# Kernel optimization log

Hardware: AMD Instinct MI355X
Metric: run time of the kernel (lower is better)

## Reference

```python
import jax, jax.numpy as jnp
import numpy as np

B, N, DIM = 8, 512, 768
H, DH = 12, 64
INNER = H * DH
MLP = 3072
DEPTH = 4
EPS = 1e-5
LS = 0.1  # LayerScale init_eps for depth <= 18


def _ln(x, scale):
    # flax LayerNorm(use_bias=False): (x-mean)/sqrt(var+eps) * scale
    mu = jnp.mean(x, axis=-1, keepdims=True)
    var = jnp.mean(jnp.square(x - mu), axis=-1, keepdims=True)
    return (x - mu) * jax.lax.rsqrt(var + EPS) * scale


def setup_inputs() -> dict:
    key = jax.random.key(0)
    ks = jax.random.split(key, 13)
    s = 0.02
    inp = {
        "x": jax.random.normal(ks[0], (B, N, DIM), jnp.float32),
        "ln1": jnp.ones((DEPTH, DIM), jnp.float32),
        "Wq": jax.random.normal(ks[1], (DEPTH, DIM, INNER), jnp.float32) * s,
        "Wkv": jax.random.normal(ks[2], (DEPTH, DIM, 2 * INNER), jnp.float32) * s,
        "mix_pre": jax.random.normal(ks[3], (DEPTH, H, H), jnp.float32) * 0.1,
        "mix_post": jax.random.normal(ks[4], (DEPTH, H, H), jnp.float32) * 0.1,
        "Wo": jax.random.normal(ks[5], (DEPTH, INNER, DIM), jnp.float32) * s,
        "bo": jnp.zeros((DEPTH, DIM), jnp.float32),
        "ln2": jnp.ones((DEPTH, DIM), jnp.float32),
        "W1": jax.random.normal(ks[6], (DEPTH, DIM, MLP), jnp.float32) * s,
        "b1": jnp.zeros((DEPTH, MLP), jnp.float32),
        "W2": jax.random.normal(ks[7], (DEPTH, MLP, DIM), jnp.float32) * s,
        "b2": jnp.zeros((DEPTH, DIM), jnp.float32),
    }
    return inp


def _block(x, p):
    ln1, Wq, Wkv, mp, mq, Wo, bo, ln2, W1, b1, W2, b2 = p
    scale = DH ** -0.5
    h = _ln(x, ln1)
    q = h @ Wq                                  # [b,n,inner]
    kv = h @ Wkv
    k, v = jnp.split(kv, 2, axis=-1)
    def to_heads(t):
        return t.reshape(B, N, H, DH).transpose(0, 2, 1, 3)  # b h n d
    q, k, v = to_heads(q), to_heads(k), to_heads(v)
    dots = jnp.einsum('bhid,bhjd->bhij', q, k) * scale
    dots = jnp.einsum('bhij,hg->bgij', dots, mp)   # talking-heads pre-softmax
    attn = jax.nn.softmax(dots, axis=-1)
    attn = jnp.einsum('bhij,hg->bgij', attn, mq)   # talking-heads post-softmax
    o = jnp.einsum('bhij,bhjd->bhid', attn, v)
    o = o.transpose(0, 2, 1, 3).reshape(B, N, INNER)
    x = (o @ Wo + bo) * LS + x
    h2 = _ln(x, ln2)
    x = ((jax.nn.gelu(h2 @ W1 + b1) @ W2) + b2) * LS + x
    return x, None


def reference(x, ln1, Wq, Wkv, mix_pre, mix_post, Wo, bo, ln2, W1, b1, W2, b2):
    params = (ln1, Wq, Wkv, mix_pre, mix_post, Wo, bo, ln2, W1, b1, W2, b2)
    out, _ = jax.lax.scan(_block, x, params)
    return out
```

## Files before the change

### kernel.cpp

```cpp
#include <hip/hip_runtime.h>


#define LSCALE 0.1f

typedef __bf16 bf16;
typedef __bf16 bf16x8 __attribute__((ext_vector_type(8)));
typedef __bf16 bf16x4 __attribute__((ext_vector_type(4)));
typedef unsigned short ushort4v __attribute__((ext_vector_type(4)));
typedef float  f32x4  __attribute__((ext_vector_type(4)));

__device__ __forceinline__ void g2l16(const void* g, void* l) {
    __builtin_amdgcn_global_load_lds(
        (const __attribute__((address_space(1))) void*)g,
        (__attribute__((address_space(3))) void*)l, 16, 0, 0);
}

template<int EPI, bool PLANA = false>
__global__ __launch_bounds__(256, 2)
void gemm_bt(const bf16* __restrict__ A, int lda, long saz1, long saz2,
             const bf16* __restrict__ Bt, int ldb, long sbz1, long sbz2,
             void* __restrict__ Cv, int ldc, long scz1, long scz2,
             int M, int N, int K, int zmod,
             const float* __restrict__ bias, float scale)
{
    __shared__ __align__(16) char smem[35840];
    bf16* As = (bf16*)smem;
    bf16* Bs = (bf16*)(smem + 16384);
    bf16* Cs = (bf16*)smem;

    const int z  = blockIdx.z;
    const int z1 = z / zmod, z2 = z - z1 * zmod;
    const bf16* Ab = A  + saz1 * (long)z1 + saz2 * (long)z2;
    const bf16* Bb = Bt + sbz1 * (long)z1 + sbz2 * (long)z2;

    const int m0 = blockIdx.x * 128, n0 = blockIdx.y * 128;
    const int tid = threadIdx.x, w = tid >> 6, l = tid & 63;
    const int wr = (w >> 1) * 64, wc = (w & 1) * 64;
    const int lr = l & 15, lq = l >> 4;
    const int srow = l >> 2, scol8 = (l & 3) * 8;

    long abase = 0;
    if constexpr (PLANA)
        abase = (long)(m0 >> 9) * 393216 + (long)((m0 & 511) + w * 32) * 64;

    f32x4 acc[4][4];
#pragma unroll
    for (int i = 0; i < 4; i++)
#pragma unroll
        for (int j = 0; j < 4; j++)
#pragma unroll
            for (int r = 0; r < 4; r++) acc[i][j][r] = 0.f;

    for (int k0 = 0; k0 < K; k0 += 64) {
        const bf16* Ag;
        int ldaa;
        if constexpr (PLANA) {
            Ag = Ab + abase + ((long)(k0 >> 6)) * 32768;
            ldaa = 64;
        } else {
            Ag = Ab + (long)(m0 + w * 32) * lda + k0;
            ldaa = lda;
        }
        const bf16* Bg = Bb + (long)(n0 + w * 32) * ldb + k0;
        g2l16(Ag + (long)srow * ldaa + scol8,             As + w * 1024);
        g2l16(Ag + (long)(srow + 16) * ldaa + scol8,      As + w * 1024 + 512);
        g2l16(Ag + (long)srow * ldaa + 32 + scol8,        As + 4096 + w * 1024);
        g2l16(Ag + (long)(srow + 16) * ldaa + 32 + scol8, As + 4096 + w * 1024 + 512);
        g2l16(Bg + (long)srow * ldb + scol8,             Bs + w * 1024);
        g2l16(Bg + (long)(srow + 16) * ldb + scol8,      Bs + w * 1024 + 512);
        g2l16(Bg + (long)srow * ldb + 32 + scol8,        Bs + 4096 + w * 1024);
        g2l16(Bg + (long)(srow + 16) * ldb + 32 + scol8, Bs + 4096 + w * 1024 + 512);
        __syncthreads();

#pragma unroll
        for (int hh = 0; hh < 2; hh++) {
            bf16x8 fa[4], fb[4];
#pragma unroll
            for (int i = 0; i < 4; i++)
                fa[i] = *(const bf16x8*)(As + hh * 4096 + (wr + i * 16 + lr) * 32 + lq * 8);
#pragma unroll
            for (int i = 0; i < 4; i++)
                fb[i] = *(const bf16x8*)(Bs + hh * 4096 + (wc + i * 16 + lr) * 32 + lq * 8);
#pragma unroll
            for (int mi = 0; mi < 4; mi++)
#pragma unroll
                for (int ni = 0; ni < 4; ni++)
                    acc[mi][ni] = __builtin_amdgcn_mfma_f32_16x16x32_bf16(
                        fa[mi], fb[ni], acc[mi][ni], 0, 0, 0);
        }
        __syncthreads();
    }

#pragma unroll
    for (int ni = 0; ni < 4; ni++) {
        const int col = wc + ni * 16 + lr;
        float bv = 0.f;
        if (EPI == 1) bv = bias[n0 + col];
#pragma unroll
        for (int mi = 0; mi < 4; mi++) {
#pragma unroll
            for (int r = 0; r < 4; r++) {
                const int row = wr + mi * 16 + lq * 4 + r;
                float v = acc[mi][ni][r];
                if (EPI == 0) {
                    v *= scale;
                } else if (EPI == 1) {
                    const float xx = v + bv;
                    const float u  = 0.7978845608f * (xx + 0.044715f * xx * xx * xx);
                    const float th = 1.f - 2.f / (__expf(2.f * u) + 1.f);
                    v = 0.5f * xx * (1.f + th);
                }
                Cs[row * 136 + col] = (bf16)v;
            }
        }
    }
    __syncthreads();

    const long cb = scz1 * (long)z1 + scz2 * (long)z2;
    const int rrow = tid >> 4, cg = tid & 15;
#pragma unroll
    for (int p = 0; p < 8; p++) {
        const int row = p * 16 + rrow;
        const bf16x8 v = *(const bf16x8*)(Cs + row * 136 + cg * 8);
        *(bf16x8*)((bf16*)Cv + cb + (long)(m0 + row) * ldc + n0 + cg * 8) = v;
    }
}

template<int PLANO>
__global__ __launch_bounds__(256, 4)
void gemm_av(const bf16* __restrict__ S, const bf16* __restrict__ qkvc,
             bf16* __restrict__ oc)
{
    __shared__ __align__(16) char av_smem[9728];
    bf16* As  = (bf16*)av_smem;
    bf16* Bst = (bf16*)(av_smem + 4096);
    bf16* Cs  = (bf16*)av_smem;

    const int z = blockIdx.y, b = z / 12, g = z - b * 12;
    const bf16* Ab = S + (long)z * 262144;
    const bf16* Bb = qkvc + (long)b * 1179648 + 1536 + g * 64;

    const int i0 = blockIdx.x * 64;
    const int tid = threadIdx.x, w = tid >> 6, l = tid & 63;
    const int lr = l & 15, lq = l >> 4;
    const int srow = l >> 2, scol8 = (l & 3) * 8;
    const int kp = tid >> 4, dq = tid & 15;
    const int kcol = ((((kp >> 2) ^ ((dq >> 1) & 3)) << 3) | ((kp & 3) << 1));

    f32x4 acc[4];
#pragma unroll
    for (int j = 0; j < 4; j++)
#pragma unroll
        for (int r = 0; r < 4; r++) acc[j][r] = 0.f;

    unsigned short* Bw = (unsigned short*)Bst;

    for (int k0 = 0; k0 < 512; k0 += 32) {
        const bf16* Ag = Ab + (long)(i0 + w * 16) * 512 + k0;
        g2l16(Ag + (long)srow * 512 + scol8, As + w * 512);

        const bf16* Bg = Bb + (long)(k0 + 2 * kp) * 2304 + dq * 4;
        ushort4v u0 = *(const ushort4v*)(Bg);
        ushort4v u1 = *(const ushort4v*)(Bg + 2304);
#pragma unroll
        for (int r = 0; r < 4; r++) {
            unsigned p = (unsigned)u0[r] | ((unsigned)u1[r] << 16);
            *(unsigned*)(Bw + (dq * 4 + r) * 40 + kcol) = p;
        }
        __syncthreads();

        bf16x8 fa = *(const bf16x8*)(As + (w * 16 + lr) * 32 + lq * 8);
        bf16x8 fb[4];
#pragma unroll
        for (int i = 0; i < 4; i++) {
            const int d = i * 16 + lr;
            fb[i] = *(const bf16x8*)(Bst + d * 40 + ((lq ^ ((d >> 3) & 3)) << 3));
        }
#pragma unroll
        for (int ni = 0; ni < 4; ni++)
            acc[ni] = __builtin_amdgcn_mfma_f32_16x16x32_bf16(
                fa, fb[ni], acc[ni], 0, 0, 0);
        __syncthreads();
    }

    if constexpr (PLANO) {
#pragma unroll
        for (int ni = 0; ni < 4; ni++)
#pragma unroll
            for (int r = 0; r < 4; r++)
                Cs[(w * 16 + lq * 4 + r) * 68 + ni * 16 + lr] = (bf16)acc[ni][r];
        __syncthreads();
        const int rr = tid >> 2, c16 = (tid & 3) * 16;
        bf16* orow = oc + ((long)z * 512 + i0 + rr) * 64 + c16;
        *(bf16x8*)(orow)     = *(const bf16x8*)(Cs + rr * 68 + c16);
        *(bf16x8*)(orow + 8) = *(const bf16x8*)(Cs + rr * 68 + c16 + 8);
    } else {
        bf16* Cb = oc + (long)b * 1179648 + g * 64;
#pragma unroll
        for (int ni = 0; ni < 4; ni++) {
            const int gc = ni * 16 + lr;
#pragma unroll
            for (int r = 0; r < 4; r++) {
                const int gr = i0 + w * 16 + lq * 4 + r;
                Cb[(long)gr * 2304 + gc] = (bf16)acc[ni][r];
            }
        }
    }
}

__global__ __launch_bounds__(256)
void tconv_k(const float* __restrict__ in, bf16* __restrict__ out,
             int K, int N)
{
    __shared__ float t[32][33];
    const int n0 = blockIdx.x * 32, k0 = blockIdx.y * 32;
    const int x = threadIdx.x, y = threadIdx.y;
#pragma unroll
    for (int yy = 0; yy < 4; yy++)
        t[y + yy * 8][x] = in[(long)(k0 + y + yy * 8) * N + n0 + x];
    __syncthreads();
#pragma unroll
    for (int yy = 0; yy < 4; yy++)
        out[(long)(n0 + y + yy * 8) * K + k0 + x] = (bf16)t[x][y + yy * 8];
}

__global__ __launch_bounds__(256)
void pre_k(const float* __restrict__ Wq, const float* __restrict__ Wkv,
           const float* __restrict__ Wo, const float* __restrict__ W1,
           const float* __restrict__ W2, bf16* __restrict__ WtAll,
           const float* __restrict__ x, float* __restrict__ xf,
           const float* __restrict__ gam, bf16* __restrict__ hout)
{
    __shared__ __align__(16) char pmem[16640];
    const int bxg = blockIdx.x;
    const int t = threadIdx.x;
    if (bxg < 6912) {
        float (*st)[65] = (float(*)[65])pmem;
        const int L = bxg / 1728;
        int bx = bxg - L * 1728;
        bf16* WtL = WtAll + (long)L * 7077888;
        const float* src; bf16* dst; int K, N, ntn;
        if (bx < 144) {
            src = Wq + (long)L * 589824;   dst = WtL;            K = 768;  N = 768;  ntn = 12;
        } else if (bx < 432) {
            bx -= 144;
            src = Wkv + (long)L * 1179648; dst = WtL + 589824;   K = 768;  N = 1536; ntn = 24;
        } else if (bx < 576) {
            bx -= 432;
            src = Wo + (long)L * 589824;   dst = WtL + 1769472;  K = 768;  N = 768;  ntn = 12;
        } else if (bx < 1152) {
            bx -= 576;
            src = W1 + (long)L * 2359296;  dst = WtL + 2359296;  K = 768;  N = 3072; ntn = 48;
        } else {
            bx -= 1152;
            src = W2 + (long)L * 2359296;  dst = WtL + 4718592;  K = 3072; N = 768;  ntn = 12;
        }
        const int n0 = (bx % ntn) * 64, k0 = (bx / ntn) * 64;
        const int r = t >> 4, c4 = (t & 15) * 4;
#pragma unroll
        for (int rr = 0; rr < 4; rr++) {
            const f32x4 v = *(const f32x4*)(src + (long)(k0 + r + rr * 16) * N + n0 + c4);
            st[r + rr * 16][c4 + 0] = v[0];
            st[r + rr * 16][c4 + 1] = v[1];
            st[r + rr * 16][c4 + 2] = v[2];
            st[r + rr * 16][c4 + 3] = v[3];
        }
        __syncthreads();
        const int kc = (t & 7) * 8;
#pragma unroll
        for (int p = 0; p < 2; p++) {
            const int n = p * 32 + (t >> 3);
            bf16x8 o;
#pragma unroll
            for (int e = 0; e < 8; e++) o[e] = (bf16)st[kc + e][n];
            *(bf16x8*)(dst + (long)(n0 + n) * K + k0 + kc) = o;
        }
    } else {
        const int row = bxg - 6912;
        float* ps  = (float*)pmem;
        float* pss = (float*)pmem + 4;
        const float* xin = x + (long)row * 768;
        float* xr = xf + (long)row * 768;
        float v[3];
#pragma unroll
        for (int i = 0; i < 3; i++) {
            const int c = t + i * 256;
            const float xv = xin[c];
            xr[c] = xv;
            v[i] = xv;
        }
        float s  = v[0] + v[1] + v[2];
        float ss = v[0] * v[0] + v[1] * v[1] + v[2] * v[2];
#pragma unroll
        for (int off = 32; off; off >>= 1) {
            s  += __shfl_xor(s, off);
            ss += __shfl_xor(ss, off);
        }
        const int wv = t >> 6, l = t & 63;
        if (l == 0) { ps[wv] = s; pss[wv] = ss; }
        __syncthreads();
        s  = ps[0] + ps[1] + ps[2] + ps[3];
        ss = pss[0] + pss[1] + pss[2] + pss[3];
        const float mu = s * (1.f / 768.f);
        const float rs = rsqrtf(ss * (1.f / 768.f) - mu * mu + 1e-5f);
        bf16* orow = hout + (long)row * 768;
#pragma unroll
        for (int i = 0; i < 3; i++) {
            const int c = t + i * 256;
            orow[c] = (bf16)((v[i] - mu) * rs * gam[c]);
        }
    }
}

__global__ __launch_bounds__(256)
void lnres_k(float* __restrict__ xf, const bf16* __restrict__ P0,
             const bf16* __restrict__ P1, const float* __restrict__ bias,
             const float* __restrict__ gam, bf16* __restrict__ out,
             const float* __restrict__ src)
{
    const int row = blockIdx.x, t = threadIdx.x;
    float* xr = xf + (long)row * 768;
    float v[3];
#pragma unroll
    for (int i = 0; i < 3; i++) {
        const int c = t + i * 256;
        float xv;
        if (src) {
            xv = src[(long)row * 768 + c];
            xr[c] = xv;
        } else if (P0) {
            xv = xr[c] + LSCALE * ((float)P0[(long)row * 768 + c] +
                                   (float)P1[(long)row * 768 + c] + bias[c]);
            xr[c] = xv;
        } else {
            xv = xr[c];
        }
        v[i] = xv;
    }
    float s  = v[0] + v[1] + v[2];
    float ss = v[0] * v[0] + v[1] * v[1] + v[2] * v[2];
#pragma unroll
    for (int off = 32; off; off >>= 1) {
        s  += __shfl_xor(s, off);
        ss += __shfl_xor(ss, off);
    }
    __shared__ float ps[4], pss[4];
    const int wv = t >> 6, l = t & 63;
    if (l == 0) { ps[wv] = s; pss[wv] = ss; }
    __syncthreads();
    s  = ps[0] + ps[1] + ps[2] + ps[3];
    ss = pss[0] + pss[1] + pss[2] + pss[3];
    const float mu = s * (1.f / 768.f);
    const float rs = rsqrtf(ss * (1.f / 768.f) - mu * mu + 1e-5f);
    bf16* orow = out + (long)row * 768;
#pragma unroll
    for (int i = 0; i < 3; i++) {
        const int c = t + i * 256;
        orow[c] = (bf16)((v[i] - mu) * rs * gam[c]);
    }
}

__global__ __launch_bounds__(256)
void outres_k(const float* __restrict__ xf, const bf16* __restrict__ P0,
              const bf16* __restrict__ P1, const float* __restrict__ bias,
              float* __restrict__ out)
{
    const long i4 = ((long)blockIdx.x * 256 + threadIdx.x) * 4;
    const int c = (int)(i4 % 768);
    const f32x4 xv = *(const f32x4*)(xf + i4);
    const bf16x4 p0 = *(const bf16x4*)(P0 + i4);
    const bf16x4 p1 = *(const bf16x4*)(P1 + i4);
    const f32x4 bv = *(const f32x4*)(bias + c);
    f32x4 o;
#pragma unroll
    for (int e = 0; e < 4; e++)
        o[e] = xv[e] + LSCALE * ((float)p0[e] + (float)p1[e] + bv[e]);
    *(f32x4*)(out + i4) = o;
}

__global__ __launch_bounds__(256)
void mixsm_k(bf16* __restrict__ S, const float* __restrict__ mp,
             const float* __restrict__ mq)
{
    const int b = blockIdx.y, i4 = blockIdx.x, t = threadIdx.x;
    const int w = t >> 6, l = t & 63;
    const int row = i4 * 4 + w;
    bf16* Sb = S + ((long)b * 12 * 512 + row) * 512 + l * 8;

    float a[12][8];
#pragma unroll
    for (int g = 0; g < 12; g++)
#pragma unroll
        for (int e = 0; e < 8; e++) a[g][e] = 0.f;

#pragma unroll
    for (int h = 0; h < 12; h++) {
        const bf16x8 sv = *(const bf16x8*)(Sb + (long)h * 262144);
        float f[8];
#pragma unroll
        for (int e = 0; e < 8; e++) f[e] = (float)sv[e];
#pragma unroll
        for (int g = 0; g < 12; g++) {
            const float m = mp[h * 12 + g];
#pragma unroll
            for (int e = 0; e < 8; e++) a[g][e] += f[e] * m;
        }
    }

#pragma unroll
    for (int g = 0; g < 12; g++) {
        float mx = a[g][0];
#pragma unroll
        for (int e = 1; e < 8; e++) mx = fmaxf(mx, a[g][e]);
#pragma unroll
        for (int off = 32; off; off >>= 1) mx = fmaxf(mx, __shfl_xor(mx, off));
        float sm = 0.f;
#pragma unroll
        for (int e = 0; e < 8; e++) {
            const float ev = __expf(a[g][e] - mx);
            a[g][e] = ev;
            sm += ev;
        }
#pragma unroll
        for (int off = 32; off; off >>= 1) sm += __shfl_xor(sm, off);
        const float rd = 1.f / sm;
#pragma unroll
        for (int e = 0; e < 8; e++) a[g][e] *= rd;
    }

#pragma unroll
    for (int hf = 0; hf < 2; hf++) {
        float o[6][8];
#pragma unroll
        for (int gg = 0; gg < 6; gg++)
#pragma unroll
            for (int e = 0; e < 8; e++) o[gg][e] = 0.f;
#pragma unroll
        for (int h = 0; h < 12; h++) {
#pragma unroll
            for (int gg = 0; gg < 6; gg++) {
                const float m = mq[h * 12 + hf * 6 + gg];
#pragma unroll
                for (int e = 0; e < 8; e++) o[gg][e] += a[h][e] * m;
            }
        }
#pragma unroll
        for (int gg = 0; gg < 6; gg++) {
            bf16x8 ov;
#pragma unroll
            for (int e = 0; e < 8; e++) ov[e] = (bf16)o[gg][e];
            *(bf16x8*)(Sb + (long)(hf * 6 + gg) * 262144) = ov;
        }
    }
}

extern "C" void kernel_launch(void* const* d_in, const int* in_sizes, int n_in,
                              void* d_out, int out_size, void* d_ws, size_t ws_size,
                              hipStream_t stream)
{
    (void)in_sizes; (void)n_in; (void)out_size;
    const float* x   = (const float*)d_in[0];
    const float* ln1 = (const float*)d_in[1];
    const float* Wq  = (const float*)d_in[2];
    const float* Wkv = (const float*)d_in[3];
    const float* mp  = (const float*)d_in[4];
    const float* mq  = (const float*)d_in[5];
    const float* Wo  = (const float*)d_in[6];
    const float* bo  = (const float*)d_in[7];
    const float* ln2 = (const float*)d_in[8];
    const float* W1  = (const float*)d_in[9];
    const float* b1  = (const float*)d_in[10];
    const float* W2  = (const float*)d_in[11];
    const float* b2  = (const float*)d_in[12];

    char* ws = (char*)d_ws;
    float* xf  = (float*)(ws);
    bf16* h    = (bf16*)(ws + 12582912);
    bf16* qkv  = (bf16*)(ws + 18874368);
    bf16* S    = (bf16*)(ws + 37748736);
    bf16* mid  = S;
    bf16* P0   = h;
    bf16* P1w2 = qkv;
    bf16* P1wo = S;
    const long P1W2_OFF = 3145728;
    const long P1WO_OFF = 12582912;

    const dim3 tb(32, 8);

    if (ws_size >= 150994944ull) {
        bf16* WtAll = (bf16*)(ws + 88080384);
        bf16* oP    = (bf16*)(ws + 144703488);

        pre_k<<<11008, 256, 0, stream>>>(Wq, Wkv, Wo, W1, W2, WtAll,
                                         x, xf, ln1, h);

        for (int L = 0; L < 4; L++) {
            bf16* WtL = WtAll + (long)L * 7077888;

            if (L > 0)
                lnres_k<<<4096, 256, 0, stream>>>(xf, P0, P1w2, b2 + (L - 1) * 768,
                                                  ln1 + L * 768, h, nullptr);

            gemm_bt<0><<<dim3(32, 18, 1), 256, 0, stream>>>(
                h, 768, 0, 0, WtL, 768, 0, 0,
                qkv, 2304, 0, 0, 4096, 2304, 768, 1, nullptr, 1.f);

            gemm_bt<0><<<dim3(4, 4, 96), 256, 0, stream>>>(
                qkv,       2304, 1179648, 64,
                qkv + 768, 2304, 1179648, 64,
                S,          512, 3145728, 262144,
                512, 512, 64, 12, nullptr, 0.125f);

            mixsm_k<<<dim3(128, 8), 256, 0, stream>>>(S, mp + L * 144, mq + L * 144);

            gemm_av<1><<<dim3(8, 96), 256, 0, stream>>>(S, qkv, oP);

            gemm_bt<4, true><<<dim3(32, 6, 2), 256, 0, stream>>>(
                oP, 64, 0, 196608, WtL + 1769472, 768, 0, 384,
                P0, 768, 0, P1WO_OFF, 4096, 768, 384, 2, nullptr, 1.f);

            lnres_k<<<4096, 256, 0, stream>>>(xf, P0, P1wo, bo + L * 768,
                                              ln2 + L * 768, h, nullptr);

            gemm_bt<1><<<dim3(32, 24, 1), 256, 0, stream>>>(
                h, 768, 0, 0, WtL + 2359296, 768, 0, 0,
                mid, 3072, 0, 0, 4096, 3072, 768, 1, b1 + L * 3072, 1.f);

            gemm_bt<4><<<dim3(32, 6, 2), 256, 0, stream>>>(
                mid, 3072, 0, 1536, WtL + 4718592, 3072, 0, 1536,
                P0, 768, 0, P1W2_OFF, 4096, 768, 1536, 2, nullptr, 1.f);
        }
    } else {
        bf16* Wt = (bf16*)(ws + 62914560);

        for (int L = 0; L < 4; L++) {
            tconv_k<<<dim3(24, 24), tb, 0, stream>>>(Wq + (long)L * 589824, Wt, 768, 768);
            tconv_k<<<dim3(48, 24), tb, 0, stream>>>(Wkv + (long)L * 1179648, Wt + 589824, 768, 1536);

            if (L == 0)
                lnres_k<<<4096, 256, 0, stream>>>(xf, nullptr, nullptr, nullptr,
                                                  ln1 + L * 768, h, x);
            else
                lnres_k<<<4096, 256, 0, stream>>>(xf, P0, P1w2, b2 + (L - 1) * 768,
                                                  ln1 + L * 768, h, nullptr);

            gemm_bt<0><<<dim3(32, 18, 1), 256, 0, stream>>>(
                h, 768, 0, 0, Wt, 768, 0, 0,
                qkv, 2304, 0, 0, 4096, 2304, 768, 1, nullptr, 1.f);

            for (int c = 0; c < 2; c++) {
                const long qb = (long)c * 4718592;
                gemm_bt<0><<<dim3(4, 4, 48), 256, 0, stream>>>(
                    qkv + qb,       2304, 1179648, 64,
                    qkv + 768 + qb, 2304, 1179648, 64,
                    S,               512, 3145728, 262144,
                    512, 512, 64, 12, nullptr, 0.125f);

                mixsm_k<<<dim3(128, 4), 256, 0, stream>>>(S, mp + L * 144, mq + L * 144);

                gemm_av<0><<<dim3(8, 48), 256, 0, stream>>>(S, qkv + qb, qkv + qb);
            }

            tconv_k<<<dim3(24, 24), tb, 0, stream>>>(Wo + (long)L * 589824, Wt, 768, 768);
            gemm_bt<4><<<dim3(32, 6, 2), 256, 0, stream>>>(
                qkv, 2304, 0, 384, Wt, 768, 0, 384,
                P0, 768, 0, P1WO_OFF, 4096, 768, 384, 2, nullptr, 1.f);

            lnres_k<<<4096, 256, 0, stream>>>(xf, P0, P1wo, bo + L * 768,
                                              ln2 + L * 768, h, nullptr);

            tconv_k<<<dim3(96, 24), tb, 0, stream>>>(W1 + (long)L * 2359296, Wt, 768, 3072);
            gemm_bt<1><<<dim3(32, 24, 1), 256, 0, stream>>>(
                h, 768, 0, 0, Wt, 768, 0, 0,
                mid, 3072, 0, 0, 4096, 3072, 768, 1, b1 + L * 3072, 1.f);

            tconv_k<<<dim3(24, 96), tb, 0, stream>>>(W2 + (long)L * 2359296, Wt, 3072, 768);
            gemm_bt<4><<<dim3(32, 6, 2), 256, 0, stream>>>(
                mid, 3072, 0, 1536, Wt, 3072, 0, 1536,
                P0, 768, 0, P1W2_OFF, 4096, 768, 1536, 2, nullptr, 1.f);
        }
    }

    outres_k<<<3072, 256, 0, stream>>>(xf, P0, P1w2, b2 + 3 * 768, (float*)d_out);
}
```

Baseline: 910.4 us.

## Interleave heads in score layout and rework talking-heads softmax kernel

Stores the QK^T scores as [b][i][h][j], with the 12 heads of one query row adjacent, so the talking-heads mixing kernel reads and writes contiguous 12x512 chunks. The av GEMM is changed to read that strided layout. mixsm_k now handles one query row per block, keeps the mixed logits in shared memory, and splits the softmax across waves instead of holding 96 floats per thread. The aim is lower register pressure and better memory locality, at the cost of extra LDS traffic, two block barriers, and a strided A load in the av GEMM.

```diff
diff --git a/kernel.cpp b/kernel.cpp
--- a/kernel.cpp
+++ b/kernel.cpp
@@ -137,7 +137,15 @@
     bf16* Cs  = (bf16*)av_smem;
 
     const int z = blockIdx.y, b = z / 12, g = z - b * 12;
-    const bf16* Ab = S + (long)z * 262144;
+    const bf16* Ab;
+    int sld;
+    if constexpr (PLANO) {
+        Ab = S + (long)b * 3145728 + g * 512;
+        sld = 6144;
+    } else {
+        Ab = S + (long)z * 262144;
+        sld = 512;
+    }
     const bf16* Bb = qkvc + (long)b * 1179648 + 1536 + g * 64;
 
     const int i0 = blockIdx.x * 64;
@@ -156,8 +164,8 @@
     unsigned short* Bw = (unsigned short*)Bst;
 
     for (int k0 = 0; k0 < 512; k0 += 32) {
-        const bf16* Ag = Ab + (long)(i0 + w * 16) * 512 + k0;
-        g2l16(Ag + (long)srow * 512 + scol8, As + w * 512);
+        const bf16* Ag = Ab + (long)(i0 + w * 16) * sld + k0;
+        g2l16(Ag + (long)srow * sld + scol8, As + w * 512);
 
         const bf16* Bg = Bb + (long)(k0 + 2 * kp) * 2304 + dq * 4;
         ushort4v u0 = *(const ushort4v*)(Bg);
@@ -378,79 +386,80 @@
     *(f32x4*)(out + i4) = o;
 }
 
+template<int CONTIG>
 __global__ __launch_bounds__(256)
 void mixsm_k(bf16* __restrict__ S, const float* __restrict__ mp,
              const float* __restrict__ mq)
 {
-    const int b = blockIdx.y, i4 = blockIdx.x, t = threadIdx.x;
-    const int w = t >> 6, l = t & 63;
-    const int row = i4 * 4 + w;
-    bf16* Sb = S + ((long)b * 12 * 512 + row) * 512 + l * 8;
-
-    float a[12][8];
-#pragma unroll
-    for (int g = 0; g < 12; g++)
-#pragma unroll
-        for (int e = 0; e < 8; e++) a[g][e] = 0.f;
-
+    __shared__ float buf[12][512];
+    __shared__ float rds[12];
+    const int b = blockIdx.y, i = blockIdx.x, t = threadIdx.x;
+    const long pstr = CONTIG ? 512 : 262144;
+    bf16* Sb = CONTIG ? S + ((long)b * 512 + i) * 6144
+                      : S + ((long)b * 12 * 512 + i) * 512;
+
+    float s0[12], s1[12];
 #pragma unroll
     for (int h = 0; h < 12; h++) {
-        const bf16x8 sv = *(const bf16x8*)(Sb + (long)h * 262144);
-        float f[8];
-#pragma unroll
-        for (int e = 0; e < 8; e++) f[e] = (float)sv[e];
-#pragma unroll
-        for (int g = 0; g < 12; g++) {
+        union { unsigned u; bf16 v[2]; } p;
+        p.u = *(const unsigned*)(Sb + h * pstr + 2 * t);
+        s0[h] = (float)p.v[0];
+        s1[h] = (float)p.v[1];
+    }
+#pragma unroll
+    for (int g = 0; g < 12; g++) {
+        float a0 = 0.f, a1 = 0.f;
+#pragma unroll
+        for (int h = 0; h < 12; h++) {
             const float m = mp[h * 12 + g];
-#pragma unroll
-            for (int e = 0; e < 8; e++) a[g][e] += f[e] * m;
-        }
-    }
-
-#pragma unroll
-    for (int g = 0; g < 12; g++) {
-        float mx = a[g][0];
-#pragma unroll
-        for (int e = 1; e < 8; e++) mx = fmaxf(mx, a[g][e]);
+            a0 += s0[h] * m;
+            a1 += s1[h] * m;
+        }
+        *(float2*)(&buf[g][2 * t]) = make_float2(a0, a1);
+    }
+    __syncthreads();
+
+    const int wv = t >> 6, l = t & 63;
+    for (int g = wv; g < 12; g += 4) {
+        float mx = -3.0e38f;
+#pragma unroll
+        for (int k = 0; k < 8; k++) mx = fmaxf(mx, buf[g][l + 64 * k]);
 #pragma unroll
         for (int off = 32; off; off >>= 1) mx = fmaxf(mx, __shfl_xor(mx, off));
         float sm = 0.f;
 #pragma unroll
-        for (int e = 0; e < 8; e++) {
-            const float ev = __expf(a[g][e] - mx);
-            a[g][e] = ev;
-            sm += ev;
+        for (int k = 0; k < 8; k++) {
+            const float e = __expf(buf[g][l + 64 * k] - mx);
+            buf[g][l + 64 * k] = e;
+            sm += e;
         }
 #pragma unroll
         for (int off = 32; off; off >>= 1) sm += __shfl_xor(sm, off);
-        const float rd = 1.f / sm;
-#pragma unroll
-        for (int e = 0; e < 8; e++) a[g][e] *= rd;
-    }
-
-#pragma unroll
-    for (int hf = 0; hf < 2; hf++) {
-        float o[6][8];
-#pragma unroll
-        for (int gg = 0; gg < 6; gg++)
-#pragma unroll
-            for (int e = 0; e < 8; e++) o[gg][e] = 0.f;
+        if (l == 0) rds[g] = 1.f / sm;
+    }
+    __syncthreads();
+
+    float e0[12], e1[12];
+#pragma unroll
+    for (int h = 0; h < 12; h++) {
+        const float2 ee = *(const float2*)(&buf[h][2 * t]);
+        const float rd = rds[h];
+        e0[h] = ee.x * rd;
+        e1[h] = ee.y * rd;
+    }
+#pragma unroll
+    for (int g = 0; g < 12; g++) {
+        float a0 = 0.f, a1 = 0.f;
 #pragma unroll
         for (int h = 0; h < 12; h++) {
-#pragma unroll
-            for (int gg = 0; gg < 6; gg++) {
-                const float m = mq[h * 12 + hf * 6 + gg];
-#pragma unroll
-                for (int e = 0; e < 8; e++) o[gg][e] += a[h][e] * m;
-            }
-        }
-#pragma unroll
-        for (int gg = 0; gg < 6; gg++) {
-            bf16x8 ov;
-#pragma unroll
-            for (int e = 0; e < 8; e++) ov[e] = (bf16)o[gg][e];
-            *(bf16x8*)(Sb + (long)(hf * 6 + gg) * 262144) = ov;
-        }
+            const float m = mq[h * 12 + g];
+            a0 += e0[h] * m;
+            a1 += e1[h] * m;
+        }
+        union { unsigned u; bf16 v[2]; } p;
+        p.v[0] = (bf16)a0;
+        p.v[1] = (bf16)a1;
+        *(unsigned*)(Sb + g * pstr + 2 * t) = p.u;
     }
 }
 
@@ -508,10 +517,10 @@
             gemm_bt<0><<<dim3(4, 4, 96), 256, 0, stream>>>(
                 qkv,       2304, 1179648, 64,
                 qkv + 768, 2304, 1179648, 64,
-                S,          512, 3145728, 262144,
+                S,         6144, 3145728, 512,
                 512, 512, 64, 12, nullptr, 0.125f);
 
-            mixsm_k<<<dim3(128, 8), 256, 0, stream>>>(S, mp + L * 144, mq + L * 144);
+            mixsm_k<1><<<dim3(512, 8), 256, 0, stream>>>(S, mp + L * 144, mq + L * 144);
 
             gemm_av<1><<<dim3(8, 96), 256, 0, stream>>>(S, qkv, oP);
 
@@ -556,7 +565,7 @@
                     S,               512, 3145728, 262144,
                     512, 512, 64, 12, nullptr, 0.125f);
 
-                mixsm_k<<<dim3(128, 4), 256, 0, stream>>>(S, mp + L * 144, mq + L * 144);
+                mixsm_k<0><<<dim3(512, 4), 256, 0, stream>>>(S, mp + L * 144, mq + L * 144);
 
                 gemm_av<0><<<dim3(8, 48), 256, 0, stream>>>(S, qkv + qb, qkv + qb);
             }
```

Result: faster. 872.3 us (-4.2%).
